# Performance work log

Hardware: AMD Instinct MI355X
Metric: run time of the kernel (lower is better)

The kernel has to match this reference:

```python
import jax, jax.numpy as jnp
import numpy as np
import math

B, T, C = 2, 2048, 2048
NH = 16
HS = C // NH            # 128
N_ELEM = int(0.5 * HS)  # 64, rotary_percentage=0.5
A_T = 10                # adapter_prompt_length


def setup_inputs() -> dict:
    key = jax.random.key(0)
    ks = jax.random.split(key, 8)
    x = jax.random.normal(ks[0], (B, T, C), dtype=jnp.float32)
    # RoPE cache: standard cos/sin of shape (T, n_elem)
    theta = 10000.0 ** (-jnp.arange(0, N_ELEM, 2, dtype=jnp.float32) / N_ELEM)
    pos = jnp.arange(T, dtype=jnp.float32)
    ang = pos[:, None] * theta[None, :]           # (T, n_elem/2)
    ang = jnp.concatenate([ang, ang], axis=-1)    # (T, n_elem)
    cos, sin = jnp.cos(ang), jnp.sin(ang)
    mask = jnp.tril(jnp.ones((T, T), dtype=bool))  # causal
    s = 0.02
    attn_w = jax.random.normal(ks[1], (3 * C, C), dtype=jnp.float32) * s
    attn_b = jax.random.normal(ks[2], (3 * C,), dtype=jnp.float32) * s
    proj_w = jax.random.normal(ks[3], (C, C), dtype=jnp.float32) * s
    proj_b = jax.random.normal(ks[4], (C,), dtype=jnp.float32) * s
    adapter_wte = jax.random.normal(ks[5], (A_T, C), dtype=jnp.float32) * s
    gating_factor = jnp.full((1,), 0.1, dtype=jnp.float32)  # nonzero so adapter path matters
    return {"x": x, "cos": cos, "sin": sin, "mask": mask,
            "attn_w": attn_w, "attn_b": attn_b, "proj_w": proj_w, "proj_b": proj_b,
            "adapter_wte": adapter_wte, "gating_factor": gating_factor}


def apply_rope(t, cos, sin):
    # t: (B, nh, T, n_elem); cos/sin: (T, n_elem)
    half = t.shape[-1] // 2
    t1, t2 = t[..., :half], t[..., half:]
    rotated = jnp.concatenate([-t2, t1], axis=-1)
    return t * cos + rotated * sin


def sdpa(q, k, v, mask, scale):
    # q: (B,nh,Tq,hs), k/v: (B,nh,Tk,hs); mask: bool broadcastable to (Tq,Tk) or None
    s = jnp.einsum('bhqd,bhkd->bhqk', q, k) * scale
    if mask is not None:
        s = jnp.where(mask, s, jnp.finfo(s.dtype).min)
    p = jax.nn.softmax(s, axis=-1)
    return jnp.einsum('bhqk,bhkd->bhqd', p, v)


def reference(x, cos, sin, mask, attn_w, attn_b, proj_w, proj_b, adapter_wte, gating_factor):
    scale = 1.0 / math.sqrt(HS)
    qkv = x @ attn_w.T + attn_b                    # (B,T,3C)
    qkv = qkv.reshape(B, T, NH, 3 * HS).transpose(0, 2, 1, 3)  # (B,nh,T,3hs)
    q, k, v = jnp.split(qkv, 3, axis=-1)           # each (B,nh,T,hs)
    q = jnp.concatenate([apply_rope(q[..., :N_ELEM], cos, sin), q[..., N_ELEM:]], axis=-1)
    k = jnp.concatenate([apply_rope(k[..., :N_ELEM], cos, sin), k[..., N_ELEM:]], axis=-1)
    y = sdpa(q, k, v, mask, scale)                 # (B,nh,T,hs)
    # adapter-prefix attention
    a_qkv = adapter_wte @ attn_w.T + attn_b        # (aT, 3C)
    _, ak, av = jnp.split(a_qkv, 3, axis=-1)       # (aT, C) each
    ak = ak.reshape(1, A_T, NH, HS).transpose(0, 2, 1, 3)  # (1,nh,aT,hs)
    av = av.reshape(1, A_T, NH, HS).transpose(0, 2, 1, 3)
    ak = jnp.broadcast_to(ak, (B, NH, A_T, HS))
    av = jnp.broadcast_to(av, (B, NH, A_T, HS))
    ay = sdpa(q, ak, av, None, scale)              # full (no mask)
    y = y + gating_factor * ay
    y = y.transpose(0, 2, 1, 3).reshape(B, T, C)
    return y @ proj_w.T + proj_b
```

## Files before the change

kernel.cpp:

```cpp
#include <hip/hip_runtime.h>
#include <math.h>

#define B_DIM 2
#define T_DIM 2048
#define C_DIM 2048
#define NHEAD 16
#define HS 128
#define QKV_N 6144
#define AT 10
#define M_DIM 4096

using bf16x8 = __attribute__((ext_vector_type(8))) short;
using f32x4v = __attribute__((ext_vector_type(4))) float;

__device__ __forceinline__ unsigned short f2bf(float f) {
    union { float f; unsigned int u; } cv; cv.f = f;
    unsigned int u = cv.u;
    return (unsigned short)((u + 0x7FFFu + ((u >> 16) & 1u)) >> 16);
}
__device__ __forceinline__ float bf2f(unsigned short h) {
    union { unsigned int u; float f; } cv; cv.u = ((unsigned int)h) << 16;
    return cv.f;
}
__device__ __forceinline__ unsigned int pack_bf16(float lo, float hi) {
    unsigned int r;
    asm volatile("v_cvt_pk_bf16_f32 %0, %1, %2" : "=v"(r) : "v"(lo), "v"(hi));
    return r;
}
__device__ __forceinline__ void gload_lds16(const void* g, void* l) {
    __builtin_amdgcn_global_load_lds(
        (const __attribute__((address_space(1))) void*)g,
        (__attribute__((address_space(3))) void*)l, 16, 0, 0);
}

__global__ __launch_bounds__(256)
void f32_to_bf16_kernel(const float* __restrict__ in, unsigned short* __restrict__ out, int n8) {
    const int i = blockIdx.x * 256 + threadIdx.x;
    if (i >= n8) return;
    const float4 a = *(const float4*)&in[(size_t)i * 8];
    const float4 b = *(const float4*)&in[(size_t)i * 8 + 4];
    *(ushort4*)&out[(size_t)i * 8]     = make_ushort4(f2bf(a.x), f2bf(a.y), f2bf(a.z), f2bf(a.w));
    *(ushort4*)&out[(size_t)i * 8 + 4] = make_ushort4(f2bf(b.x), f2bf(b.y), f2bf(b.z), f2bf(b.w));
}

template<int BF16OUT>
__global__ __launch_bounds__(256)
void gemm_nt_mfma(const unsigned short* __restrict__ A, const unsigned short* __restrict__ Bw,
                  const float* __restrict__ bias, void* __restrict__ Cout,
                  int M, int N, int K) {
    __shared__ unsigned short As[128 * 32];
    __shared__ unsigned short Bs[128 * 32];

    const int tid  = threadIdx.x;
    const int wave = tid >> 6;
    const int lane = tid & 63;

    const int nwg = gridDim.x * gridDim.y;
    int bid = blockIdx.y * gridDim.x + blockIdx.x;
    bid = (bid & 7) * (nwg >> 3) + (bid >> 3);
    const int m0 = (bid / gridDim.x) * 128;
    const int n0 = (bid % gridDim.x) * 128;

    const int wr = (wave >> 1) * 64;
    const int wc = (wave & 1) * 64;

    f32x4v acc[4][4];
#pragma unroll
    for (int i = 0; i < 4; ++i)
#pragma unroll
        for (int j = 0; j < 4; ++j)
#pragma unroll
            for (int q = 0; q < 4; ++q) acc[i][j][q] = 0.f;

    const int srow = lane >> 2;
    const int sk   = (lane & 3) * 8;
    const int fr   = lane & 15;
    const int fk   = (lane >> 4) * 8;

    for (int k0 = 0; k0 < K; k0 += 32) {
        __syncthreads();
#pragma unroll
        for (int t = 0; t < 2; ++t) {
            const int seg = wave * 2 + t;
            gload_lds16(&A[(size_t)(m0 + seg * 16 + srow) * K + k0 + sk], &As[seg * 512]);
            gload_lds16(&Bw[(size_t)(n0 + seg * 16 + srow) * K + k0 + sk], &Bs[seg * 512]);
        }
        __syncthreads();

        bf16x8 af[4], bfg[4];
#pragma unroll
        for (int i = 0; i < 4; ++i)
            af[i] = *(const bf16x8*)&As[(wr + i * 16 + fr) * 32 + fk];
#pragma unroll
        for (int j = 0; j < 4; ++j)
            bfg[j] = *(const bf16x8*)&Bs[(wc + j * 16 + fr) * 32 + fk];
#pragma unroll
        for (int i = 0; i < 4; ++i)
#pragma unroll
            for (int j = 0; j < 4; ++j)
                acc[i][j] = __builtin_amdgcn_mfma_f32_16x16x32_bf16(af[i], bfg[j], acc[i][j], 0, 0, 0);
    }

    const int r4 = (lane >> 4) * 4;
#pragma unroll
    for (int i = 0; i < 4; ++i) {
#pragma unroll
        for (int j = 0; j < 4; ++j) {
            const int col = n0 + wc + j * 16 + fr;
            const float bv = bias[col];
#pragma unroll
            for (int q = 0; q < 4; ++q) {
                const int row = m0 + wr + i * 16 + r4 + q;
                const float v = acc[i][j][q] + bv;
                if (BF16OUT) ((unsigned short*)Cout)[(size_t)row * N + col] = f2bf(v);
                else         ((float*)Cout)[(size_t)row * N + col] = v;
            }
        }
    }
}

__global__ __launch_bounds__(256)
void rope_repack(const unsigned short* __restrict__ qkvb, const float* __restrict__ cosb,
                 const float* __restrict__ sinb, unsigned short* __restrict__ Qb,
                 unsigned short* __restrict__ Kb, unsigned short* __restrict__ Vt) {
    __shared__ unsigned short Vlds[64 * 132];

    const int tid = threadIdx.x;
    const int t64 = blockIdx.x & 31;
    const int h   = (blockIdx.x >> 5) & 15;
    const int b   = blockIdx.x >> 9;
    const int bh  = b * NHEAD + h;
    const int t0  = t64 * 64;

    const int r = tid >> 2, part = tid & 3;
    const size_t inrow  = ((size_t)(b * T_DIM + t0 + r)) * QKV_N + h * 384;
    const size_t outrow = ((size_t)bh * T_DIM + t0 + r) * HS;

    {
        const int isK = part >> 1;
        const int sub = part & 1;
        const unsigned short* src = qkvb + inrow + isK * 128;
        unsigned short* dst = (isK ? Kb : Qb) + outrow;
        if (sub == 0) {
#pragma unroll
            for (int g = 0; g < 8; ++g) {
                const int i = g * 4;
                ushort4 t1 = *(const ushort4*)&src[i];
                ushort4 t2 = *(const ushort4*)&src[32 + i];
                const float4 cv = *(const float4*)&cosb[(t0 + r) * 64 + i];
                const float4 sv = *(const float4*)&sinb[(t0 + r) * 64 + i];
                const float a0 = bf2f(t1.x), a1 = bf2f(t1.y), a2 = bf2f(t1.z), a3 = bf2f(t1.w);
                const float b0 = bf2f(t2.x), b1 = bf2f(t2.y), b2 = bf2f(t2.z), b3 = bf2f(t2.w);
                *(ushort4*)&dst[i] = make_ushort4(
                    f2bf(a0 * cv.x - b0 * sv.x), f2bf(a1 * cv.y - b1 * sv.y),
                    f2bf(a2 * cv.z - b2 * sv.z), f2bf(a3 * cv.w - b3 * sv.w));
                *(ushort4*)&dst[32 + i] = make_ushort4(
                    f2bf(b0 * cv.x + a0 * sv.x), f2bf(b1 * cv.y + a1 * sv.y),
                    f2bf(b2 * cv.z + a2 * sv.z), f2bf(b3 * cv.w + a3 * sv.w));
            }
        } else {
#pragma unroll
            for (int g = 0; g < 8; ++g) {
                *(ushort4*)&dst[64 + g * 8]     = *(const ushort4*)&src[64 + g * 8];
                *(ushort4*)&dst[64 + g * 8 + 4] = *(const ushort4*)&src[64 + g * 8 + 4];
            }
        }
    }

    {
        const unsigned short* vsrc = qkvb + inrow + 256;
#pragma unroll
        for (int g = 0; g < 8; ++g)
            *(ushort4*)&Vlds[r * 132 + part * 32 + g * 4] = *(const ushort4*)&vsrc[part * 32 + g * 4];
    }
    __syncthreads();
    {
        const int d = tid >> 1, tc = tid & 1;
        unsigned short* vdst = Vt + ((size_t)bh * HS + d) * T_DIM + t0 + tc * 32;
#pragma unroll
        for (int g = 0; g < 8; ++g) {
            ushort4 o;
            o.x = Vlds[(tc * 32 + g * 4 + 0) * 132 + d];
            o.y = Vlds[(tc * 32 + g * 4 + 1) * 132 + d];
            o.z = Vlds[(tc * 32 + g * 4 + 2) * 132 + d];
            o.w = Vlds[(tc * 32 + g * 4 + 3) * 132 + d];
            *(ushort4*)&vdst[g * 4] = o;
        }
    }
}

__global__ __launch_bounds__(64)
void adapter_qkv_kernel(const float* __restrict__ wte, const unsigned short* __restrict__ wb,
                        const float* __restrict__ bias, float* __restrict__ aqkv) {
    const int n = blockIdx.x;
    const int lane = threadIdx.x;
    float acc[AT];
#pragma unroll
    for (int a = 0; a < AT; ++a) acc[a] = 0.f;
    for (int k = lane * 8; k < C_DIM; k += 64 * 8) {
        const ushort4 wa = *(const ushort4*)&wb[(size_t)n * C_DIM + k];
        const ushort4 wc = *(const ushort4*)&wb[(size_t)n * C_DIM + k + 4];
        const float w0 = bf2f(wa.x), w1 = bf2f(wa.y), w2 = bf2f(wa.z), w3 = bf2f(wa.w);
        const float w4 = bf2f(wc.x), w5 = bf2f(wc.y), w6 = bf2f(wc.z), w7 = bf2f(wc.w);
#pragma unroll
        for (int a = 0; a < AT; ++a) {
            const float4 t0 = *(const float4*)&wte[(size_t)a * C_DIM + k];
            const float4 t1 = *(const float4*)&wte[(size_t)a * C_DIM + k + 4];
            acc[a] += w0 * t0.x + w1 * t0.y + w2 * t0.z + w3 * t0.w
                    + w4 * t1.x + w5 * t1.y + w6 * t1.z + w7 * t1.w;
        }
    }
#pragma unroll
    for (int a = 0; a < AT; ++a) {
        float v = acc[a];
        for (int off = 32; off; off >>= 1) v += __shfl_down(v, off);
        if (lane == 0) aqkv[(size_t)a * QKV_N + n] = v + bias[n];
    }
}

__global__ __launch_bounds__(256)
void flash_mfma(const unsigned short* __restrict__ Qb, const unsigned short* __restrict__ Kb,
                const unsigned short* __restrict__ Vt, const float* __restrict__ aqkv,
                const float* __restrict__ gating, unsigned short* __restrict__ yb) {
    __shared__ __align__(16) unsigned short smem[2][16384];

    const int tid = threadIdx.x;
    const int wave = tid >> 6, lane = tid & 63;
    const int lo = lane & 15, hi = lane >> 4;

    const int z = blockIdx.x & 15;
    const int h = (blockIdx.x >> 4) & 15;
    const int b = blockIdx.x >> 8;
    const int bh = b * NHEAD + h;
    const float kscale = 0.08838834764831845f * 1.4426950408889634f;

    const unsigned short* Qh = Qb + (size_t)bh * T_DIM * HS;
    const unsigned short* Kh = Kb + (size_t)bh * T_DIM * HS;
    const unsigned short* Vh = Vt + (size_t)bh * HS * T_DIM;

    float* AK = (float*)&smem[0][0];
    float* AV = AK + AT * HS;

    auto STAGE = [&](int k0, int bufi) {
        unsigned short* Kd = &smem[bufi][0];
        unsigned short* Vd = &smem[bufi][8192];
#pragma unroll
        for (int t = 0; t < 4; ++t) {
            const int kr = wave * 16 + t * 4 + hi;
            gload_lds16(Kh + (size_t)(k0 + kr) * HS + 8 * (lo ^ (kr & 7)),
                        &Kd[(wave * 16 + t * 4) * 128]);
            const int vr = (wave * 4 + t) * 8 + (lane >> 3);
            gload_lds16(Vh + (size_t)vr * T_DIM + k0 + 8 * ((lane & 7) ^ (vr & 7)),
                        &Vd[(wave * 4 + t) * 8 * 64]);
        }
    };

#pragma unroll 1
    for (int pass = 0; pass < 2; ++pass) {
        const int qt = pass ? z : (31 - z);
        const int q0 = qt * 64;
        const int myqrow = q0 + wave * 16 + lo;

        bf16x8 qf[4];
        {
            const unsigned short* qrow = Qh + (size_t)myqrow * HS;
#pragma unroll
            for (int c = 0; c < 4; ++c) qf[c] = *(const bf16x8*)&qrow[c * 32 + hi * 8];
        }

        f32x4v oacc[8];
#pragma unroll
        for (int d = 0; d < 8; ++d)
#pragma unroll
            for (int q = 0; q < 4; ++q) oacc[d][q] = 0.f;
        float m = -INFINITY, ln = 0.f;

        STAGE(0, 0);
        int cur = 0;
        for (int kt = 0; kt <= qt; ++kt) {
            const int k0 = kt * 64;
            __syncthreads();
            if (kt < qt) STAGE(k0 + 64, cur ^ 1);
            const unsigned short* Ks = &smem[cur][0];
            const unsigned short* Vs = &smem[cur][8192];

            f32x4v sacc[4];
            __builtin_amdgcn_s_setprio(1);
#pragma unroll
            for (int s = 0; s < 4; ++s) {
#pragma unroll
                for (int q = 0; q < 4; ++q) sacc[s][q] = 0.f;
                const int krow = s * 16 + lo;
                const int rs = (lo & 7) << 4;
#pragma unroll
                for (int c = 0; c < 4; ++c) {
                    const int boff = (c * 64 + hi * 16) ^ rs;
                    bf16x8 kf = *(const bf16x8*)&Ks[krow * 128 + (boff >> 1)];
                    sacc[s] = __builtin_amdgcn_mfma_f32_16x16x32_bf16(kf, qf[c], sacc[s], 0, 0, 0);
                }
            }
            __builtin_amdgcn_s_setprio(0);

            const bool dtile = (kt == qt);
            float p[4][4];
            float xm = -INFINITY;
#pragma unroll
            for (int s = 0; s < 4; ++s)
#pragma unroll
                for (int q = 0; q < 4; ++q) {
                    float v = sacc[s][q] * kscale;
                    if (dtile && (k0 + s * 16 + hi * 4 + q > myqrow)) v = -INFINITY;
                    p[s][q] = v;
                    xm = fmaxf(xm, v);
                }
            xm = fmaxf(xm, __shfl_xor(xm, 16));
            xm = fmaxf(xm, __shfl_xor(xm, 32));
            if (__any(xm > m + 11.5f)) {
                const float mnew = fmaxf(m, xm);
                const float al = exp2f(m - mnew);
                m = mnew;
                ln *= al;
                float aq[4];
#pragma unroll
                for (int q = 0; q < 4; ++q) aq[q] = __shfl(al, hi * 4 + q);
#pragma unroll
                for (int d = 0; d < 8; ++d)
#pragma unroll
                    for (int q = 0; q < 4; ++q) oacc[d][q] *= aq[q];
            }
            float psum = 0.f;
#pragma unroll
            for (int s = 0; s < 4; ++s)
#pragma unroll
                for (int q = 0; q < 4; ++q) {
                    p[s][q] = exp2f(p[s][q] - m);
                    psum += p[s][q];
                }
            psum += __shfl_xor(psum, 16);
            psum += __shfl_xor(psum, 32);
            ln += psum;

            unsigned int pk[4][2];
#pragma unroll
            for (int s = 0; s < 4; ++s) {
                pk[s][0] = pack_bf16(p[s][0], p[s][1]);
                pk[s][1] = pack_bf16(p[s][2], p[s][3]);
            }
            const int src0 = lo + ((hi & 1) << 5);
            const int src1 = src0 + 16;
            const bool shi = (hi >> 1) != 0;
#pragma unroll
            for (int c = 0; c < 2; ++c) {
                const unsigned int a0 = (unsigned int)__shfl((int)pk[c*2][0], src0);
                const unsigned int b0 = (unsigned int)__shfl((int)pk[c*2+1][0], src0);
                const unsigned int a1 = (unsigned int)__shfl((int)pk[c*2][1], src0);
                const unsigned int b1 = (unsigned int)__shfl((int)pk[c*2+1][1], src0);
                const unsigned int a2 = (unsigned int)__shfl((int)pk[c*2][0], src1);
                const unsigned int b2 = (unsigned int)__shfl((int)pk[c*2+1][0], src1);
                const unsigned int a3 = (unsigned int)__shfl((int)pk[c*2][1], src1);
                const unsigned int b3 = (unsigned int)__shfl((int)pk[c*2+1][1], src1);
                union { unsigned int u[4]; bf16x8 v; } cv2;
                cv2.u[0] = shi ? b0 : a0;
                cv2.u[1] = shi ? b1 : a1;
                cv2.u[2] = shi ? b2 : a2;
                cv2.u[3] = shi ? b3 : a3;
                const bf16x8 pf = cv2.v;
                __builtin_amdgcn_s_setprio(1);
#pragma unroll
                for (int d = 0; d < 8; ++d) {
                    const int vrow = d * 16 + lo;
                    const int boff = (c * 64 + hi * 16) ^ ((lo & 7) << 4);
                    bf16x8 vf = *(const bf16x8*)&Vs[vrow * 64 + (boff >> 1)];
                    oacc[d] = __builtin_amdgcn_mfma_f32_16x16x32_bf16(pf, vf, oacc[d], 0, 0, 0);
                }
                __builtin_amdgcn_s_setprio(0);
            }
            cur ^= 1;
        }

        float linv[4];
#pragma unroll
        for (int q = 0; q < 4; ++q) linv[q] = 1.f / __shfl(ln, hi * 4 + q);
#pragma unroll
        for (int d = 0; d < 8; ++d)
#pragma unroll
            for (int q = 0; q < 4; ++q) oacc[d][q] *= linv[q];

        __syncthreads();
        for (int idx = tid; idx < AT * HS; idx += 256) {
            const int a = idx >> 7, d = idx & 127;
            AK[idx] = aqkv[(size_t)a * QKV_N + C_DIM + h * HS + d];
            AV[idx] = aqkv[(size_t)a * QKV_N + 2 * C_DIM + h * HS + d];
        }
        __syncthreads();

        float qflt[4][8];
#pragma unroll
        for (int c = 0; c < 4; ++c)
#pragma unroll
            for (int j = 0; j < 8; ++j) qflt[c][j] = bf2f((unsigned short)qf[c][j]);

        float e[AT];
        float amax = -INFINITY;
#pragma unroll
        for (int a = 0; a < AT; ++a) {
            float t = 0.f;
#pragma unroll
            for (int c = 0; c < 4; ++c) {
                const float4 k0v = *(const float4*)&AK[a * HS + c * 32 + hi * 8];
                const float4 k1v = *(const float4*)&AK[a * HS + c * 32 + hi * 8 + 4];
                t += qflt[c][0] * k0v.x + qflt[c][1] * k0v.y + qflt[c][2] * k0v.z + qflt[c][3] * k0v.w
                   + qflt[c][4] * k1v.x + qflt[c][5] * k1v.y + qflt[c][6] * k1v.z + qflt[c][7] * k1v.w;
            }
            t += __shfl_xor(t, 16);
            t += __shfl_xor(t, 32);
            e[a] = t * 0.08838834764831845f;
            amax = fmaxf(amax, e[a]);
        }
        float asum = 0.f;
#pragma unroll
        for (int a = 0; a < AT; ++a) { e[a] = __expf(e[a] - amax); asum += e[a]; }
        const float gcoef = gating[0] / asum;

#pragma unroll
        for (int a = 0; a < AT; ++a) {
            const float ca = e[a] * gcoef;
            float cq[4];
#pragma unroll
            for (int q = 0; q < 4; ++q) cq[q] = __shfl(ca, hi * 4 + q);
#pragma unroll
            for (int d = 0; d < 8; ++d) {
                const float av = AV[a * HS + d * 16 + lo];
#pragma unroll
                for (int q = 0; q < 4; ++q) oacc[d][q] += cq[q] * av;
            }
        }

#pragma unroll
        for (int q = 0; q < 4; ++q) {
            const int row = q0 + wave * 16 + hi * 4 + q;
            unsigned short* dst = yb + ((size_t)(b * T_DIM + row)) * C_DIM + h * HS + lo;
#pragma unroll
            for (int d = 0; d < 8; ++d) dst[d * 16] = f2bf(oacc[d][q]);
        }

        if (pass == 0) __syncthreads();
    }
}

extern "C" void kernel_launch(void* const* d_in, const int* in_sizes, int n_in,
                              void* d_out, int out_size, void* d_ws, size_t ws_size,
                              hipStream_t stream) {
    const float* x       = (const float*)d_in[0];
    const float* cosb    = (const float*)d_in[1];
    const float* sinb    = (const float*)d_in[2];
    const float* attn_w  = (const float*)d_in[4];
    const float* attn_b  = (const float*)d_in[5];
    const float* proj_w  = (const float*)d_in[6];
    const float* proj_b  = (const float*)d_in[7];
    const float* wte     = (const float*)d_in[8];
    const float* gating  = (const float*)d_in[9];
    float* out = (float*)d_out;

    float* aqkv = (float*)d_ws;
    unsigned short* qkvb = (unsigned short*)(aqkv + (size_t)AT * QKV_N);
    unsigned short* xb   = qkvb + (size_t)M_DIM * QKV_N;
    unsigned short* awb  = xb + (size_t)M_DIM * C_DIM;
    unsigned short* Vt   = awb + (size_t)QKV_N * C_DIM;
    unsigned short* Qb   = xb;
    unsigned short* Kb   = awb;
    unsigned short* pwb  = qkvb;
    unsigned short* yv   = qkvb + (size_t)C_DIM * C_DIM;

    f32_to_bf16_kernel<<<(M_DIM * C_DIM / 8 + 255) / 256, 256, 0, stream>>>(x, xb, M_DIM * C_DIM / 8);
    f32_to_bf16_kernel<<<(QKV_N * C_DIM / 8 + 255) / 256, 256, 0, stream>>>(attn_w, awb, QKV_N * C_DIM / 8);
    gemm_nt_mfma<1><<<dim3(QKV_N / 128, M_DIM / 128), 256, 0, stream>>>(
        xb, awb, attn_b, qkvb, M_DIM, QKV_N, C_DIM);
    adapter_qkv_kernel<<<QKV_N, 64, 0, stream>>>(wte, awb, attn_b, aqkv);
    rope_repack<<<B_DIM * NHEAD * (T_DIM / 64), 256, 0, stream>>>(qkvb, cosb, sinb, Qb, Kb, Vt);
    f32_to_bf16_kernel<<<(C_DIM * C_DIM / 8 + 255) / 256, 256, 0, stream>>>(proj_w, pwb, C_DIM * C_DIM / 8);
    flash_mfma<<<B_DIM * NHEAD * 16, 256, 0, stream>>>(Qb, Kb, Vt, aqkv, gating, yv);
    gemm_nt_mfma<0><<<dim3(C_DIM / 128, M_DIM / 128), 256, 0, stream>>>(
        yv, pwb, proj_b, out, M_DIM, C_DIM, C_DIM);
}
```

Before: 490.7 us.

## Pipeline GEMM with triple-buffered LDS and fuse RoPE/repack into QKV epilogue

Replaces the single-buffered GEMM with a triple-buffered global-to-LDS pipeline that uses explicit waitcnt, XOR-swizzled LDS addressing to avoid bank conflicts, and raised priority around the MFMA block. The QKV GEMM epilogue now applies bias and RoPE and writes Q, K and transposed V directly, which removes the separate rope_repack kernel and the bf16 QKV intermediate round trip. The block index mapping is reworked for tile grouping, and workspace buffers are laid out without aliasing. In exchange, the epilogue stores are narrower and scattered (2-byte stores for RoPE, strided writes for V), and the kernel uses more LDS.

After: 440.2 us. -10.3%, faster.

```diff
diff --git a/kernel.cpp b/kernel.cpp
--- a/kernel.cpp
+++ b/kernel.cpp
@@ -43,148 +43,156 @@
     *(ushort4*)&out[(size_t)i * 8 + 4] = make_ushort4(f2bf(b.x), f2bf(b.y), f2bf(b.z), f2bf(b.w));
 }
 
-template<int BF16OUT>
+template<int FUSED>
 __global__ __launch_bounds__(256)
-void gemm_nt_mfma(const unsigned short* __restrict__ A, const unsigned short* __restrict__ Bw,
-                  const float* __restrict__ bias, void* __restrict__ Cout,
-                  int M, int N, int K) {
-    __shared__ unsigned short As[128 * 32];
-    __shared__ unsigned short Bs[128 * 32];
+void gemm_pipe(const unsigned short* __restrict__ A, const unsigned short* __restrict__ Bw,
+               const float* __restrict__ bias, float* __restrict__ Cf32,
+               const float* __restrict__ cosb, const float* __restrict__ sinb,
+               unsigned short* __restrict__ Qb, unsigned short* __restrict__ Kb,
+               unsigned short* __restrict__ Vt, int M, int N, int K) {
+    __shared__ unsigned short As[3][4096];
+    __shared__ unsigned short Bs[3][4096];
 
     const int tid  = threadIdx.x;
     const int wave = tid >> 6;
     const int lane = tid & 63;
 
-    const int nwg = gridDim.x * gridDim.y;
-    int bid = blockIdx.y * gridDim.x + blockIdx.x;
+    const int ncnt = gridDim.x, mcnt = gridDim.y;
+    const int nwg = ncnt * mcnt;
+    int bid = blockIdx.y * ncnt + blockIdx.x;
     bid = (bid & 7) * (nwg >> 3) + (bid >> 3);
-    const int m0 = (bid / gridDim.x) * 128;
-    const int n0 = (bid % gridDim.x) * 128;
+    const int mt = (bid >> 3) % mcnt;
+    const int nt = (bid / (mcnt * 8)) * 8 + (bid & 7);
+    const int m0 = mt * 128, n0 = nt * 128;
 
     const int wr = (wave >> 1) * 64;
     const int wc = (wave & 1) * 64;
-
-    f32x4v acc[4][4];
-#pragma unroll
-    for (int i = 0; i < 4; ++i)
-#pragma unroll
-        for (int j = 0; j < 4; ++j)
-#pragma unroll
-            for (int q = 0; q < 4; ++q) acc[i][j][q] = 0.f;
+    const int fr = lane & 15;
+    const int hi = lane >> 4;
 
     const int srow = lane >> 2;
-    const int sk   = (lane & 3) * 8;
-    const int fr   = lane & 15;
-    const int fk   = (lane >> 4) * 8;
-
-    for (int k0 = 0; k0 < K; k0 += 32) {
-        __syncthreads();
+    const int ssk  = 8 * ((lane & 3) ^ ((lane >> 2) & 3));
+    const int swk  = 8 * (hi ^ (fr & 3));
+
+    auto STAGE = [&](int ks, int bi) {
+        const int k0 = ks << 5;
 #pragma unroll
         for (int t = 0; t < 2; ++t) {
             const int seg = wave * 2 + t;
-            gload_lds16(&A[(size_t)(m0 + seg * 16 + srow) * K + k0 + sk], &As[seg * 512]);
-            gload_lds16(&Bw[(size_t)(n0 + seg * 16 + srow) * K + k0 + sk], &Bs[seg * 512]);
-        }
-        __syncthreads();
-
+            gload_lds16(&A[(size_t)(m0 + seg * 16 + srow) * K + k0 + ssk], &As[bi][seg * 512]);
+            gload_lds16(&Bw[(size_t)(n0 + seg * 16 + srow) * K + k0 + ssk], &Bs[bi][seg * 512]);
+        }
+    };
+
+    f32x4v acc[4][4];
+#pragma unroll
+    for (int i = 0; i < 4; ++i)
+#pragma unroll
+        for (int j = 0; j < 4; ++j)
+#pragma unroll
+            for (int q = 0; q < 4; ++q) acc[i][j][q] = 0.f;
+
+    const int nk = K >> 5;
+    STAGE(0, 0);
+    STAGE(1, 1);
+
+    for (int ks = 0; ks < nk; ++ks) {
+        if (ks < nk - 1) asm volatile("s_waitcnt vmcnt(4)" ::: "memory");
+        else             asm volatile("s_waitcnt vmcnt(0)" ::: "memory");
+        __builtin_amdgcn_sched_barrier(0);
+        __builtin_amdgcn_s_barrier();
+        asm volatile("" ::: "memory");
+        __builtin_amdgcn_sched_barrier(0);
+
+        const unsigned short* Ab = As[ks % 3];
+        const unsigned short* Bb = Bs[ks % 3];
         bf16x8 af[4], bfg[4];
 #pragma unroll
         for (int i = 0; i < 4; ++i)
-            af[i] = *(const bf16x8*)&As[(wr + i * 16 + fr) * 32 + fk];
+            af[i] = *(const bf16x8*)&Ab[(wr + i * 16 + fr) * 32 + swk];
 #pragma unroll
         for (int j = 0; j < 4; ++j)
-            bfg[j] = *(const bf16x8*)&Bs[(wc + j * 16 + fr) * 32 + fk];
+            bfg[j] = *(const bf16x8*)&Bb[(wc + j * 16 + fr) * 32 + swk];
+
+        if (ks + 2 < nk) STAGE(ks + 2, (ks + 2) % 3);
+
+        __builtin_amdgcn_s_setprio(1);
 #pragma unroll
         for (int i = 0; i < 4; ++i)
 #pragma unroll
             for (int j = 0; j < 4; ++j)
                 acc[i][j] = __builtin_amdgcn_mfma_f32_16x16x32_bf16(af[i], bfg[j], acc[i][j], 0, 0, 0);
+        __builtin_amdgcn_s_setprio(0);
     }
 
-    const int r4 = (lane >> 4) * 4;
-#pragma unroll
-    for (int i = 0; i < 4; ++i) {
-#pragma unroll
-        for (int j = 0; j < 4; ++j) {
-            const int col = n0 + wc + j * 16 + fr;
-            const float bv = bias[col];
-#pragma unroll
-            for (int q = 0; q < 4; ++q) {
-                const int row = m0 + wr + i * 16 + r4 + q;
-                const float v = acc[i][j][q] + bv;
-                if (BF16OUT) ((unsigned short*)Cout)[(size_t)row * N + col] = f2bf(v);
-                else         ((float*)Cout)[(size_t)row * N + col] = v;
-            }
-        }
-    }
-}
-
-__global__ __launch_bounds__(256)
-void rope_repack(const unsigned short* __restrict__ qkvb, const float* __restrict__ cosb,
-                 const float* __restrict__ sinb, unsigned short* __restrict__ Qb,
-                 unsigned short* __restrict__ Kb, unsigned short* __restrict__ Vt) {
-    __shared__ unsigned short Vlds[64 * 132];
-
-    const int tid = threadIdx.x;
-    const int t64 = blockIdx.x & 31;
-    const int h   = (blockIdx.x >> 5) & 15;
-    const int b   = blockIdx.x >> 9;
-    const int bh  = b * NHEAD + h;
-    const int t0  = t64 * 64;
-
-    const int r = tid >> 2, part = tid & 3;
-    const size_t inrow  = ((size_t)(b * T_DIM + t0 + r)) * QKV_N + h * 384;
-    const size_t outrow = ((size_t)bh * T_DIM + t0 + r) * HS;
-
-    {
-        const int isK = part >> 1;
-        const int sub = part & 1;
-        const unsigned short* src = qkvb + inrow + isK * 128;
-        unsigned short* dst = (isK ? Kb : Qb) + outrow;
-        if (sub == 0) {
-#pragma unroll
-            for (int g = 0; g < 8; ++g) {
-                const int i = g * 4;
-                ushort4 t1 = *(const ushort4*)&src[i];
-                ushort4 t2 = *(const ushort4*)&src[32 + i];
-                const float4 cv = *(const float4*)&cosb[(t0 + r) * 64 + i];
-                const float4 sv = *(const float4*)&sinb[(t0 + r) * 64 + i];
-                const float a0 = bf2f(t1.x), a1 = bf2f(t1.y), a2 = bf2f(t1.z), a3 = bf2f(t1.w);
-                const float b0 = bf2f(t2.x), b1 = bf2f(t2.y), b2 = bf2f(t2.z), b3 = bf2f(t2.w);
-                *(ushort4*)&dst[i] = make_ushort4(
-                    f2bf(a0 * cv.x - b0 * sv.x), f2bf(a1 * cv.y - b1 * sv.y),
-                    f2bf(a2 * cv.z - b2 * sv.z), f2bf(a3 * cv.w - b3 * sv.w));
-                *(ushort4*)&dst[32 + i] = make_ushort4(
-                    f2bf(b0 * cv.x + a0 * sv.x), f2bf(b1 * cv.y + a1 * sv.y),
-                    f2bf(b2 * cv.z + a2 * sv.z), f2bf(b3 * cv.w + a3 * sv.w));
+    const int r4 = hi * 4;
+    if constexpr (FUSED) {
+        const int part = (n0 >> 7) % 3;
+        const int head = n0 / 384;
+        const int bh   = (m0 >> 11) * NHEAD + head;
+        if (part == 2) {
+#pragma unroll
+            for (int i = 0; i < 4; ++i) {
+                const int t0v = (m0 & (T_DIM - 1)) + wr + i * 16 + r4;
+#pragma unroll
+                for (int j = 0; j < 4; ++j) {
+                    const int d = wc + j * 16 + fr;
+                    const float bv = bias[n0 + d];
+                    ushort4 o = make_ushort4(f2bf(acc[i][j][0] + bv), f2bf(acc[i][j][1] + bv),
+                                             f2bf(acc[i][j][2] + bv), f2bf(acc[i][j][3] + bv));
+                    *(ushort4*)&Vt[((size_t)bh * HS + d) * T_DIM + t0v] = o;
+                }
             }
         } else {
-#pragma unroll
-            for (int g = 0; g < 8; ++g) {
-                *(ushort4*)&dst[64 + g * 8]     = *(const ushort4*)&src[64 + g * 8];
-                *(ushort4*)&dst[64 + g * 8 + 4] = *(const ushort4*)&src[64 + g * 8 + 4];
-            }
-        }
-    }
-
-    {
-        const unsigned short* vsrc = qkvb + inrow + 256;
-#pragma unroll
-        for (int g = 0; g < 8; ++g)
-            *(ushort4*)&Vlds[r * 132 + part * 32 + g * 4] = *(const ushort4*)&vsrc[part * 32 + g * 4];
-    }
-    __syncthreads();
-    {
-        const int d = tid >> 1, tc = tid & 1;
-        unsigned short* vdst = Vt + ((size_t)bh * HS + d) * T_DIM + t0 + tc * 32;
-#pragma unroll
-        for (int g = 0; g < 8; ++g) {
-            ushort4 o;
-            o.x = Vlds[(tc * 32 + g * 4 + 0) * 132 + d];
-            o.y = Vlds[(tc * 32 + g * 4 + 1) * 132 + d];
-            o.z = Vlds[(tc * 32 + g * 4 + 2) * 132 + d];
-            o.w = Vlds[(tc * 32 + g * 4 + 3) * 132 + d];
-            *(ushort4*)&vdst[g * 4] = o;
+            unsigned short* Dst = part ? Kb : Qb;
+            if (wc == 0) {
+#pragma unroll
+                for (int i = 0; i < 4; ++i) {
+#pragma unroll
+                    for (int q = 0; q < 4; ++q) {
+                        const int t = (m0 & (T_DIM - 1)) + wr + i * 16 + r4 + q;
+                        const float* crow = &cosb[t * 64];
+                        const float* srw  = &sinb[t * 64];
+                        unsigned short* drow = &Dst[((size_t)bh * T_DIM + t) * HS];
+#pragma unroll
+                        for (int j = 0; j < 2; ++j) {
+                            const int d = j * 16 + fr;
+                            const float v1 = acc[i][j][q]     + bias[n0 + d];
+                            const float v2 = acc[i][j + 2][q] + bias[n0 + d + 32];
+                            drow[d]      = f2bf(v1 * crow[d]      - v2 * srw[d]);
+                            drow[d + 32] = f2bf(v2 * crow[d + 32] + v1 * srw[d + 32]);
+                        }
+                    }
+                }
+            } else {
+#pragma unroll
+                for (int i = 0; i < 4; ++i) {
+                    const int t0r = (m0 & (T_DIM - 1)) + wr + i * 16 + r4;
+#pragma unroll
+                    for (int j = 0; j < 4; ++j) {
+                        const int d = 64 + j * 16 + fr;
+                        const float bv = bias[n0 + d];
+                        unsigned short* dcol = &Dst[((size_t)bh * T_DIM + t0r) * HS + d];
+#pragma unroll
+                        for (int q = 0; q < 4; ++q)
+                            dcol[(size_t)q * HS] = f2bf(acc[i][j][q] + bv);
+                    }
+                }
+            }
+        }
+    } else {
+#pragma unroll
+        for (int i = 0; i < 4; ++i) {
+#pragma unroll
+            for (int j = 0; j < 4; ++j) {
+                const int col = n0 + wc + j * 16 + fr;
+                const float bv = bias[col];
+#pragma unroll
+                for (int q = 0; q < 4; ++q) {
+                    const int row = m0 + wr + i * 16 + r4 + q;
+                    Cf32[(size_t)row * N + col] = acc[i][j][q] + bv;
+                }
+            }
         }
     }
 }
@@ -463,23 +471,21 @@
     float* out = (float*)d_out;
 
     float* aqkv = (float*)d_ws;
-    unsigned short* qkvb = (unsigned short*)(aqkv + (size_t)AT * QKV_N);
-    unsigned short* xb   = qkvb + (size_t)M_DIM * QKV_N;
-    unsigned short* awb  = xb + (size_t)M_DIM * C_DIM;
-    unsigned short* Vt   = awb + (size_t)QKV_N * C_DIM;
-    unsigned short* Qb   = xb;
-    unsigned short* Kb   = awb;
-    unsigned short* pwb  = qkvb;
-    unsigned short* yv   = qkvb + (size_t)C_DIM * C_DIM;
+    unsigned short* xb  = (unsigned short*)(aqkv + (size_t)AT * QKV_N);
+    unsigned short* awb = xb  + (size_t)M_DIM * C_DIM;
+    unsigned short* Qb  = awb + (size_t)QKV_N * C_DIM;
+    unsigned short* Kb  = Qb  + (size_t)B_DIM * NHEAD * T_DIM * HS;
+    unsigned short* Vt  = Kb  + (size_t)B_DIM * NHEAD * T_DIM * HS;
+    unsigned short* pwb = Vt  + (size_t)B_DIM * NHEAD * T_DIM * HS;
+    unsigned short* yv  = pwb + (size_t)C_DIM * C_DIM;
 
     f32_to_bf16_kernel<<<(M_DIM * C_DIM / 8 + 255) / 256, 256, 0, stream>>>(x, xb, M_DIM * C_DIM / 8);
     f32_to_bf16_kernel<<<(QKV_N * C_DIM / 8 + 255) / 256, 256, 0, stream>>>(attn_w, awb, QKV_N * C_DIM / 8);
-    gemm_nt_mfma<1><<<dim3(QKV_N / 128, M_DIM / 128), 256, 0, stream>>>(
-        xb, awb, attn_b, qkvb, M_DIM, QKV_N, C_DIM);
+    gemm_pipe<1><<<dim3(QKV_N / 128, M_DIM / 128), 256, 0, stream>>>(
+        xb, awb, attn_b, nullptr, cosb, sinb, Qb, Kb, Vt, M_DIM, QKV_N, C_DIM);
     adapter_qkv_kernel<<<QKV_N, 64, 0, stream>>>(wte, awb, attn_b, aqkv);
-    rope_repack<<<B_DIM * NHEAD * (T_DIM / 64), 256, 0, stream>>>(qkvb, cosb, sinb, Qb, Kb, Vt);
     f32_to_bf16_kernel<<<(C_DIM * C_DIM / 8 + 255) / 256, 256, 0, stream>>>(proj_w, pwb, C_DIM * C_DIM / 8);
     flash_mfma<<<B_DIM * NHEAD * 16, 256, 0, stream>>>(Qb, Kb, Vt, aqkv, gating, yv);
-    gemm_nt_mfma<0><<<dim3(C_DIM / 128, M_DIM / 128), 256, 0, stream>>>(
-        yv, pwb, proj_b, out, M_DIM, C_DIM, C_DIM);
-}
+    gemm_pipe<0><<<dim3(C_DIM / 128, M_DIM / 128), 256, 0, stream>>>(
+        yv, pwb, proj_b, out, nullptr, nullptr, nullptr, nullptr, nullptr, M_DIM, C_DIM, C_DIM);
+}
```
